# Performance work log

Measured on AMD Instinct MI355X. Metric: run time of the kernel, lower is better.

## Reference

```python
import jax, jax.numpy as jnp
import numpy as np

IN, H, T = 512, 1024, 1024


def _xavier(key, shape):
    a = (6.0 / (shape[0] + shape[1])) ** 0.5
    return jax.random.uniform(key, shape, minval=-a, maxval=a, dtype=jnp.float32)


def setup_inputs() -> dict:
    key = jax.random.key(0)
    ks = jax.random.split(key, 20)
    inp = {
        'x': jax.random.normal(ks[0], (1, T, IN), dtype=jnp.float32),
        'time': jax.random.uniform(ks[1], (T,), dtype=jnp.float32),
    }
    # initial states ~ N(0, 0.1) as in the source forward
    names = ['h0_1', 'c0_1', 'h0_2', 'c0_2', 'h0_3', 'c0_3']
    for i, n in enumerate(names):
        inp[n] = 0.1 * jax.random.normal(ks[2 + i], (1, H), dtype=jnp.float32)
    # LSTMCell params: weights xavier_uniform, biases uniform(0,1) (torch gate order i,f,g,o)
    inp['W_ih1'] = _xavier(ks[8], (4 * H, IN + 1))
    inp['W_hh1'] = _xavier(ks[9], (4 * H, H))
    inp['b_ih1'] = jax.random.uniform(ks[10], (4 * H,), dtype=jnp.float32)
    inp['b_hh1'] = jax.random.uniform(ks[11], (4 * H,), dtype=jnp.float32)
    inp['W_ih2'] = _xavier(ks[12], (4 * H, H))
    inp['W_hh2'] = _xavier(ks[13], (4 * H, H))
    inp['b_ih2'] = jax.random.uniform(ks[14], (4 * H,), dtype=jnp.float32)
    inp['b_hh2'] = jax.random.uniform(ks[15], (4 * H,), dtype=jnp.float32)
    return inp


def reference(x, time, h0_1, c0_1, h0_2, c0_2, h0_3, c0_3,
              W_ih1, W_hh1, b_ih1, b_hh1, W_ih2, W_hh2, b_ih2, b_hh2):
    def cell(xt, h, c, W_ih, W_hh, b_ih, b_hh):
        gates = xt @ W_ih.T + b_ih + h @ W_hh.T + b_hh  # (1, 4H)
        i, f, g, o = jnp.split(gates, 4, axis=-1)
        c_new = jax.nn.sigmoid(f) * c + jax.nn.sigmoid(i) * jnp.tanh(g)
        h_new = jax.nn.sigmoid(o) * jnp.tanh(c_new)
        return h_new, c_new

    xs = jnp.concatenate([x[0], time[:, None]], axis=1)  # (T, IN+1)

    def step(carry, xt):
        h1, c1, h2, c2, h3, c3 = carry
        h1, c1 = cell(xt[None, :], h1, c1, W_ih1, W_hh1, b_ih1, b_hh1)
        h2, c2 = cell(h1, h2, c2, W_ih2, W_hh2, b_ih2, b_hh2)
        # source calls self.lstm2 again for the third layer (lstm3 unused)
        h3, c3 = cell(h2, h3, c3, W_ih2, W_hh2, b_ih2, b_hh2)
        return (h1, c1, h2, c2, h3, c3), h3[0]

    carry, hs = jax.lax.scan(step, (h0_1, c0_1, h0_2, c0_2, h0_3, c0_3), xs)
    hs = hs[None]              # (1, T, H)
    h_final = carry[4]         # (1, H) -- last h3
    attn = jnp.einsum('bth,bh->bt', hs, h_final)
    w = jax.nn.softmax(attn, axis=1)
    context = jnp.einsum('bth,bt->bh', hs, w)  # (1, H)
    return context
```

## Files before the change

### kernel.cpp

```cpp
#include <hip/hip_runtime.h>
#include <hip/hip_fp16.h>

#define TSTEPS 1024
#define HDIM   1024
#define INDIM  512
#define NGATE  4096
#define NWG_L1  64
#define NWG_L23 128
#define NWG_TOT 192
#define POISON_U 0x7C7C7C7Cu
#define SPIN_MAX (1 << 20)


typedef _Float16 half2v __attribute__((ext_vector_type(2)));
typedef decltype(__builtin_amdgcn_cvt_pkrtz(0.f, 0.f)) f16x2b;

#define PINU(v) asm volatile("" : "+v"(v))

#if defined(__has_builtin)
#if __has_builtin(__builtin_amdgcn_fdot2)
#define HAVE_FDOT2 1
#endif
#endif

#ifdef HAVE_FDOT2
__device__ __forceinline__ float dot2f(unsigned h, unsigned w, float c) {
    return __builtin_amdgcn_fdot2(__builtin_bit_cast(f16x2b, h),
                                  __builtin_bit_cast(f16x2b, w), c, false);
}
#else
__device__ __forceinline__ float dot2f(unsigned h, unsigned w, float c) {
    half2v a = __builtin_bit_cast(half2v, h);
    half2v b = __builtin_bit_cast(half2v, w);
    c = fmaf((float)a[0], (float)b[0], c);
    c = fmaf((float)a[1], (float)b[1], c);
    return c;
}
#endif

__device__ __forceinline__ float wave_sum64_dpp(float v) {
    int x;
    x = __builtin_amdgcn_update_dpp(0, __float_as_int(v), 0x111, 0xf, 0xf, false); v += __int_as_float(x);
    x = __builtin_amdgcn_update_dpp(0, __float_as_int(v), 0x112, 0xf, 0xf, false); v += __int_as_float(x);
    x = __builtin_amdgcn_update_dpp(0, __float_as_int(v), 0x114, 0xf, 0xf, false); v += __int_as_float(x);
    x = __builtin_amdgcn_update_dpp(0, __float_as_int(v), 0x118, 0xf, 0xf, false); v += __int_as_float(x);
    x = __builtin_amdgcn_update_dpp(0, __float_as_int(v), 0x142, 0xa, 0xf, false); v += __int_as_float(x);
    x = __builtin_amdgcn_update_dpp(0, __float_as_int(v), 0x143, 0xc, 0xf, false); v += __int_as_float(x);
    return v;
}

__device__ __forceinline__ float sigm(float x) { return 1.f / (1.f + __expf(-x)); }
__device__ __forceinline__ float fast_tanh(float x) {
    float t = __expf(-2.f * fabsf(x));
    float r = (1.f - t) / (1.f + t);
    return copysignf(r, x);
}

__device__ __forceinline__ unsigned pack_h(float a, float b) {
    auto p = __builtin_amdgcn_cvt_pkrtz(a, b);
    return __builtin_bit_cast(unsigned, p);
}

__device__ __forceinline__ unsigned agent_loadu(const unsigned* p) {
    return __hip_atomic_load(const_cast<unsigned*>(p), __ATOMIC_RELAXED,
                             __HIP_MEMORY_SCOPE_AGENT);
}
__device__ __forceinline__ void agent_storeu(unsigned* p, unsigned v) {
    __hip_atomic_store(p, v, __ATOMIC_RELAXED, __HIP_MEMORY_SCOPE_AGENT);
}
__device__ __forceinline__ float agent_loadf(const float* p) {
    return __hip_atomic_load(const_cast<float*>(p), __ATOMIC_RELAXED,
                             __HIP_MEMORY_SCOPE_AGENT);
}
__device__ __forceinline__ void agent_storef(float* p, float v) {
    __hip_atomic_store(p, v, __ATOMIC_RELAXED, __HIP_MEMORY_SCOPE_AGENT);
}
__device__ __forceinline__ bool isp(float v) { return __float_as_uint(v) == POISON_U; }

__device__ __forceinline__ void grid_barrier(int* bar, int idx, int tid) {
    __syncthreads();
    if (tid == 0) {
        __hip_atomic_fetch_add(&bar[idx], 1, __ATOMIC_ACQ_REL,
                               __HIP_MEMORY_SCOPE_AGENT);
        for (int it = 0; it < SPIN_MAX; ++it) {
            if (__hip_atomic_load(&bar[idx], __ATOMIC_ACQUIRE,
                                  __HIP_MEMORY_SCOPE_AGENT) >= NWG_TOT) break;
            __builtin_amdgcn_s_sleep(2);
        }
    }
    __syncthreads();
}

#define BM 64
#define BN 64
#define BK 32
#define GK (INDIM + 1)

__device__ __forceinline__ void gemm_tile(
    int bm, int bn, int ttid,
    const float* __restrict__ B, const float* __restrict__ bias1,
    const float* __restrict__ bias2, float* C,
    const float* __restrict__ x, const float* __restrict__ timev,
    float (*As)[BM + 1], float (*Bs)[BN + 1])
{
    const int t0 = bm * BM;
    const int n0 = bn * BN;
    const int tx = ttid & 15;
    const int ty = ttid >> 4;

    float acc[4][4] = {{0.f}};

    for (int kc = 0; kc < GK; kc += BK) {
#pragma unroll
        for (int i = 0; i < 8; i++) {
            int idx = ttid + i * 256;
            int r = idx >> 5;
            int c = idx & 31;
            int col = kc + c;
            int trow = t0 + r;
            float av = (col < INDIM) ? x[(size_t)trow * INDIM + col]
                                     : ((col == INDIM) ? timev[trow] : 0.f);
            As[c][r] = av;
            int nrow = n0 + r;
            Bs[c][r] = (col < GK) ? B[(size_t)nrow * GK + col] : 0.f;
        }
        __syncthreads();

#pragma unroll
        for (int kk = 0; kk < BK; kk++) {
            float a[4], b[4];
#pragma unroll
            for (int i = 0; i < 4; i++) a[i] = As[kk][ty * 4 + i];
#pragma unroll
            for (int j = 0; j < 4; j++) b[j] = Bs[kk][tx * 4 + j];
#pragma unroll
            for (int i = 0; i < 4; i++)
#pragma unroll
                for (int j = 0; j < 4; j++)
                    acc[i][j] = fmaf(a[i], b[j], acc[i][j]);
        }
        __syncthreads();
    }

#pragma unroll
    for (int i = 0; i < 4; i++) {
        int trow = t0 + ty * 4 + i;
#pragma unroll
        for (int j = 0; j < 4; j++) {
            int n = n0 + tx * 4 + j;
            agent_storef(C + (size_t)trow * NGATE + n,
                         acc[i][j] + bias1[n] + bias2[n]);
        }
    }
}

__global__ __launch_bounds__(1024, 4) void fused_scan(
    const float* __restrict__ Whh1,
    float* G1,
    const float* __restrict__ Wih2,
    const float* __restrict__ Whh2,
    const float* __restrict__ Wih1,
    const float* __restrict__ bih1, const float* __restrict__ bhh1,
    const float* __restrict__ xin, const float* __restrict__ timev,
    const float* bih2, const float* bhh2,
    const float* h0_1, const float* c0_1,
    const float* h0_2, const float* c0_2,
    const float* h0_3, const float* c0_3,
    unsigned* H1p, unsigned* H2p, unsigned* H3p,
    float* H3f,
    float* attnb, float* outp, int* bar)
{
    __shared__ unsigned shp1[512];
    __shared__ unsigned shp2[512];
    __shared__ unsigned shp3[512];
    __shared__ float gbuf[16][4];
    __shared__ float AsT[4][BK][BM + 1];
    __shared__ float BsT[4][BK][BN + 1];

    const int tid = threadIdx.x;
    const int wg  = blockIdx.x;
    const int q   = tid >> 6;
    const int s   = tid & 63;

    if (wg < NWG_L1) {
        const int u0 = wg << 4;
        const int u  = u0 + q;
        unsigned w[4][8];
#pragma unroll
        for (int g = 0; g < 4; ++g) {
            const float* row = Whh1 + (size_t)((g << 10) + u) * 1024 + 2 * s;
#pragma unroll
            for (int m = 0; m < 8; ++m) {
                float2 v = *(const float2*)(row + 128 * m);
                w[g][m] = pack_h(v.x, v.y);
            }
        }
        float c1 = (tid < 16) ? c0_1[u0 + tid] : 0.f;
        unsigned pv = 0u;

        for (int t = 0; t < TSTEPS; ++t) {
#pragma unroll
            for (int g = 0; g < 4; ++g)
#pragma unroll
                for (int m = 0; m < 8; ++m) PINU(w[g][m]);

            float Gv0 = 0.f, Gv1 = 0.f, Gv2 = 0.f, Gv3 = 0.f;
            if (tid < 16) {
                const float* gptr = G1 + (size_t)t * NGATE + u0 + tid;
                Gv0 = agent_loadf(gptr);
                Gv1 = agent_loadf(gptr + 1024);
                Gv2 = agent_loadf(gptr + 2048);
                Gv3 = agent_loadf(gptr + 3072);
            }
            if (tid < 512) {
                if (t == 0) {
                    shp1[tid] = pack_h(h0_1[2 * tid], h0_1[2 * tid + 1]);
                } else {
                    const unsigned* p = H1p + (size_t)(t - 1) * 512 + tid;
                    unsigned v = pv;
                    for (int it = 0; it < SPIN_MAX; ++it) {
                        if (__ballot(v == POISON_U) == 0ULL) break;
                        __builtin_amdgcn_s_sleep(1);
                        if (v == POISON_U) v = agent_loadu(p);
                    }
                    shp1[tid] = v;
                }
            }
            __syncthreads();

            float a0 = 0.f, a1 = 0.f, a2 = 0.f, a3 = 0.f;
#pragma unroll
            for (int m = 0; m < 8; ++m) {
                unsigned hu = shp1[s + 64 * m];
                a0 = dot2f(hu, w[0][m], a0);
                a1 = dot2f(hu, w[1][m], a1);
                a2 = dot2f(hu, w[2][m], a2);
                a3 = dot2f(hu, w[3][m], a3);
            }
            a0 = wave_sum64_dpp(a0);
            a1 = wave_sum64_dpp(a1);
            a2 = wave_sum64_dpp(a2);
            a3 = wave_sum64_dpp(a3);
            if (s == 63) {
                gbuf[q][0] = a0;
                gbuf[q][1] = a1;
                gbuf[q][2] = a2;
                gbuf[q][3] = a3;
            }
            __syncthreads();

            if (tid < 16) {
                const float* gptr = G1 + (size_t)t * NGATE + u0 + tid;
                for (int it = 0; it < SPIN_MAX; ++it) {
                    if (__ballot(isp(Gv0) | isp(Gv1) | isp(Gv2) | isp(Gv3)) == 0ULL)
                        break;
                    __builtin_amdgcn_s_sleep(1);
                    if (isp(Gv0)) Gv0 = agent_loadf(gptr);
                    if (isp(Gv1)) Gv1 = agent_loadf(gptr + 1024);
                    if (isp(Gv2)) Gv2 = agent_loadf(gptr + 2048);
                    if (isp(Gv3)) Gv3 = agent_loadf(gptr + 3072);
                }
                float gi = gbuf[tid][0] + Gv0;
                float gf = gbuf[tid][1] + Gv1;
                float gg = gbuf[tid][2] + Gv2;
                float go = gbuf[tid][3] + Gv3;
                float i_ = sigm(gi), f_ = sigm(gf), g_ = fast_tanh(gg), o_ = sigm(go);
                c1 = f_ * c1 + i_ * g_;
                float hn = o_ * fast_tanh(c1);
                float hnn = __shfl_down(hn, 1, 64);
                if (!(tid & 1))
                    agent_storeu(H1p + (size_t)t * 512 + (u0 >> 1) + (tid >> 1),
                                 pack_h(hn, hnn));
            }
            if (tid < 512 && t < TSTEPS - 1) {
                pv = agent_loadu(H1p + (size_t)t * 512 + tid);
                PINU(pv);
            }
        }
    } else {
        {
            const int team = tid >> 8;
            const int ttid = tid & 255;
            const int tg   = (wg - NWG_L1) * 4 + team;
#pragma unroll
            for (int r = 0; r < 2; ++r) {
                const int wk = tg + r * 512;
                gemm_tile(wk >> 6, wk & 63, ttid, Wih1, bih1, bhh1, G1,
                          xin, timev, AsT[team], BsT[team]);
            }
        }
        __syncthreads();

        const int ul = q >> 1;
        const int gp = q & 1;
        const int u0 = (wg - NWG_L1) << 3;
        const int u  = u0 + ul;
        unsigned wi[2][8], wh[2][8];
#pragma unroll
        for (int j = 0; j < 2; ++j) {
            const float* ri = Wih2 + (size_t)(((2 * gp + j) << 10) + u) * 1024 + 2 * s;
            const float* rh = Whh2 + (size_t)(((2 * gp + j) << 10) + u) * 1024 + 2 * s;
#pragma unroll
            for (int m = 0; m < 8; ++m) {
                float2 vi = *(const float2*)(ri + 128 * m);
                float2 vh = *(const float2*)(rh + 128 * m);
                wi[j][m] = pack_h(vi.x, vi.y);
                wh[j][m] = pack_h(vh.x, vh.y);
            }
        }
        float bias0 = 0.f, bias1v = 0.f, bias2v = 0.f, bias3 = 0.f, cst = 0.f;
        if (tid < 16) {
            int uu = u0 + (tid & 7);
            bias0  = bih2[uu]        + bhh2[uu];
            bias1v = bih2[1024 + uu] + bhh2[1024 + uu];
            bias2v = bih2[2048 + uu] + bhh2[2048 + uu];
            bias3  = bih2[3072 + uu] + bhh2[3072 + uu];
            cst = (tid < 8) ? c0_2[u0 + tid] : c0_3[u0 + tid - 8];
        }
        unsigned pv1 = 0u;
        if (tid < 512) pv1 = agent_loadu(H1p + tid);

        for (int t = 0; t <= TSTEPS; ++t) {
#pragma unroll
            for (int j = 0; j < 2; ++j)
#pragma unroll
                for (int m = 0; m < 8; ++m) { PINU(wi[j][m]); PINU(wh[j][m]); }

            const bool do2 = (t < TSTEPS);
            const bool do3 = (t >= 1);

            if (tid < 512 && do2) {
                const unsigned* p = H1p + (size_t)t * 512 + tid;
                unsigned v = pv1;
                for (int it = 0; it < SPIN_MAX; ++it) {
                    if (__ballot(v == POISON_U) == 0ULL) break;
                    __builtin_amdgcn_s_sleep(1);
                    if (v == POISON_U) v = agent_loadu(p);
                }
                shp1[tid] = v;
            }
            __syncthreads();

            float p20 = 0.f, p21 = 0.f;
#pragma unroll
            for (int m = 0; m < 8; ++m) {
                unsigned h1u = shp1[s + 64 * m];
                p20 = dot2f(h1u, wi[0][m], p20);
                p21 = dot2f(h1u, wi[1][m], p21);
            }

            if (tid < 512) {
                if (t == 0) {
                    shp2[tid] = pack_h(h0_2[2 * tid], h0_2[2 * tid + 1]);
                } else {
                    const unsigned* p = H2p + (size_t)(t - 1) * 512 + tid;
                    unsigned v = agent_loadu(p);
                    for (int it = 0; it < SPIN_MAX; ++it) {
                        if (__ballot(v == POISON_U) == 0ULL) break;
                        __builtin_amdgcn_s_sleep(1);
                        if (v == POISON_U) v = agent_loadu(p);
                    }
                    shp2[tid] = v;
                }
            } else {
                const int sid = tid - 512;
                if (t == 1) {
                    shp3[sid] = pack_h(h0_3[2 * sid], h0_3[2 * sid + 1]);
                } else if (t > 1) {
                    const unsigned* p = H3p + (size_t)(t - 2) * 512 + sid;
                    unsigned v = agent_loadu(p);
                    for (int it = 0; it < SPIN_MAX; ++it) {
                        if (__ballot(v == POISON_U) == 0ULL) break;
                        __builtin_amdgcn_s_sleep(1);
                        if (v == POISON_U) v = agent_loadu(p);
                    }
                    shp3[sid] = v;
                }
            }
            __syncthreads();

            float p30 = 0.f, p31 = 0.f;
#pragma unroll
            for (int m = 0; m < 8; ++m) {
                unsigned h2u = shp2[s + 64 * m];
                unsigned h3u = shp3[s + 64 * m];
                p20 = dot2f(h2u, wh[0][m], p20);
                p21 = dot2f(h2u, wh[1][m], p21);
                p30 = dot2f(h2u, wi[0][m], p30);
                p31 = dot2f(h2u, wi[1][m], p31);
                p30 = dot2f(h3u, wh[0][m], p30);
                p31 = dot2f(h3u, wh[1][m], p31);
            }
            float s20 = wave_sum64_dpp(p20);
            float s21 = wave_sum64_dpp(p21);
            float s30 = wave_sum64_dpp(p30);
            float s31 = wave_sum64_dpp(p31);
            if (s == 63) {
                gbuf[ul][2 * gp]          = s20;
                gbuf[ul][2 * gp + 1]      = s21;
                gbuf[8 + ul][2 * gp]      = s30;
                gbuf[8 + ul][2 * gp + 1]  = s31;
            }
            __syncthreads();

            if (tid < 16) {
                const bool act = (tid < 8) ? do2 : do3;
                float hn = 0.f;
                if (act) {
                    float gi = gbuf[tid][0] + bias0;
                    float gf = gbuf[tid][1] + bias1v;
                    float gg = gbuf[tid][2] + bias2v;
                    float go = gbuf[tid][3] + bias3;
                    float i_ = sigm(gi), f_ = sigm(gf), g_ = fast_tanh(gg), o_ = sigm(go);
                    cst = f_ * cst + i_ * g_;
                    hn = o_ * fast_tanh(cst);
                }
                float hnn = __shfl_down(hn, 1, 64);
                if (act) {
                    if (tid < 8) {
                        if (!(tid & 1))
                            agent_storeu(H2p + (size_t)t * 512 + (u0 >> 1) + (tid >> 1),
                                         pack_h(hn, hnn));
                    } else {
                        if (!(tid & 1))
                            agent_storeu(H3p + (size_t)(t - 1) * 512 + (u0 >> 1) + ((tid - 8) >> 1),
                                         pack_h(hn, hnn));
                        agent_storef(H3f + (size_t)(t - 1) * HDIM + u0 + (tid - 8), hn);
                    }
                }
            }
            if (tid < 512 && t < TSTEPS - 1) {
                pv1 = agent_loadu(H1p + (size_t)(t + 1) * 512 + tid);
                PINU(pv1);
            }
        }
    }

    const int gw = wg * 16 + q;
    grid_barrier(bar, 0, tid);

    if (gw < TSTEPS) {
        const float* hrow = H3f + (size_t)gw * HDIM;
        const float* hf   = H3f + (size_t)(TSTEPS - 1) * HDIM;
        float p = 0.f;
#pragma unroll
        for (int j = 0; j < 16; ++j) {
            int k = s + 64 * j;
            p = fmaf(agent_loadf(hrow + k), agent_loadf(hf + k), p);
        }
        p = wave_sum64_dpp(p);
        if (s == 63) agent_storef(attnb + gw, p);
    }
    grid_barrier(bar, 1, tid);

    if (wg == 0 && tid < 64) {
        float m = -1e30f;
        for (int i = 0; i < 16; ++i)
            m = fmaxf(m, agent_loadf(attnb + tid + i * 64));
#pragma unroll
        for (int d = 32; d; d >>= 1) m = fmaxf(m, __shfl_xor(m, d, 64));
        float ss = 0.f;
        for (int i = 0; i < 16; ++i)
            ss += __expf(agent_loadf(attnb + tid + i * 64) - m);
#pragma unroll
        for (int d = 32; d; d >>= 1) ss += __shfl_xor(ss, d, 64);
        float inv = 1.f / ss;
        for (int i = 0; i < 16; ++i) {
            int idx = tid + i * 64;
            agent_storef(attnb + idx,
                         __expf(agent_loadf(attnb + idx) - m) * inv);
        }
    }
    grid_barrier(bar, 2, tid);

    if (gw < HDIM) {
        float p = 0.f;
#pragma unroll
        for (int j = 0; j < 16; ++j) {
            int t = s + 64 * j;
            p = fmaf(agent_loadf(H3f + (size_t)t * HDIM + gw),
                     agent_loadf(attnb + t), p);
        }
        p = wave_sum64_dpp(p);
        if (s == 63) outp[gw] = p;
    }
}

extern "C" void kernel_launch(void* const* d_in, const int* in_sizes, int n_in,
                              void* d_out, int out_size, void* d_ws, size_t ws_size,
                              hipStream_t stream)
{
    const float* x     = (const float*)d_in[0];
    const float* timev = (const float*)d_in[1];
    const float* h0_1  = (const float*)d_in[2];
    const float* c0_1  = (const float*)d_in[3];
    const float* h0_2  = (const float*)d_in[4];
    const float* c0_2  = (const float*)d_in[5];
    const float* h0_3  = (const float*)d_in[6];
    const float* c0_3  = (const float*)d_in[7];
    const float* Wih1  = (const float*)d_in[8];
    const float* Whh1  = (const float*)d_in[9];
    const float* bih1  = (const float*)d_in[10];
    const float* bhh1  = (const float*)d_in[11];
    const float* Wih2  = (const float*)d_in[12];
    const float* Whh2  = (const float*)d_in[13];
    const float* bih2  = (const float*)d_in[14];
    const float* bhh2  = (const float*)d_in[15];

    float* G      = (float*)d_ws;
    unsigned* H1p = (unsigned*)(G + (size_t)TSTEPS * NGATE);
    unsigned* H2p = H1p + (size_t)TSTEPS * 512;
    unsigned* H3p = H2p + (size_t)TSTEPS * 512;
    float* H3f    = (float*)(H3p + (size_t)TSTEPS * 512);
    float* attnb  = H3f + (size_t)TSTEPS * HDIM;
    int* bar      = (int*)(attnb + 1024);
    float* out    = (float*)d_out;

    hipMemsetAsync(G, 0x7C,
                   (size_t)TSTEPS * NGATE * sizeof(float) +
                   (size_t)3 * TSTEPS * 512 * sizeof(unsigned), stream);
    hipMemsetAsync(bar, 0, 16 * sizeof(int), stream);

    {
        const float* a0 = Whh1;  float* a1 = G;
        const float* a2 = Wih2;  const float* a3 = Whh2;
        const float* a4 = Wih1;  const float* a5 = bih1;  const float* a6 = bhh1;
        const float* a7 = x;     const float* a8 = timev;
        const float* a9 = bih2;  const float* a10 = bhh2;
        const float* a11 = h0_1; const float* a12 = c0_1;
        const float* a13 = h0_2; const float* a14 = c0_2;
        const float* a15 = h0_3; const float* a16 = c0_3;
        unsigned* a17 = H1p; unsigned* a18 = H2p; unsigned* a19 = H3p;
        float* a20 = H3f; float* a21 = attnb; float* a22 = out; int* a23 = bar;
        void* args[] = {&a0,&a1,&a2,&a3,&a4,&a5,&a6,&a7,&a8,&a9,&a10,&a11,
                        &a12,&a13,&a14,&a15,&a16,&a17,&a18,&a19,&a20,&a21,
                        &a22,&a23};
        hipLaunchCooperativeKernel((void*)fused_scan, dim3(NWG_TOT), dim3(1024),
                                   args, 0, stream);
    }
}
```

Before: 2.892 ms.

## Split layer-2/3 step phases, fuse softmax into context, pad LDS tiles

Splits the layer-2 and layer-3 computation inside each timestep so layer 2's hidden state is computed and published before layer 3's dot products, which shortens the critical path for the next step's dependency. It also removes one grid barrier by having every wave redundantly compute the softmax max and sum and fold the normalisation into the context reduction. LDS tile padding changes from +1 to +4, and weight packing switches to round-to-nearest fp16. The costs are an extra __syncthreads per step and redundant softmax work in every wave.

```diff
diff --git a/kernel.cpp b/kernel.cpp
--- a/kernel.cpp
+++ b/kernel.cpp
@@ -60,6 +60,10 @@
     auto p = __builtin_amdgcn_cvt_pkrtz(a, b);
     return __builtin_bit_cast(unsigned, p);
 }
+__device__ __forceinline__ unsigned pack_rne(float a, float b) {
+    return (unsigned)__half_as_ushort(__float2half(a)) |
+           ((unsigned)__half_as_ushort(__float2half(b)) << 16);
+}
 
 __device__ __forceinline__ unsigned agent_loadu(const unsigned* p) {
     return __hip_atomic_load(const_cast<unsigned*>(p), __ATOMIC_RELAXED,
@@ -101,7 +105,7 @@
     const float* __restrict__ B, const float* __restrict__ bias1,
     const float* __restrict__ bias2, float* C,
     const float* __restrict__ x, const float* __restrict__ timev,
-    float (*As)[BM + 1], float (*Bs)[BN + 1])
+    float (*As)[BM + 4], float (*Bs)[BN + 4])
 {
     const int t0 = bm * BM;
     const int n0 = bn * BN;
@@ -174,8 +178,8 @@
     __shared__ unsigned shp2[512];
     __shared__ unsigned shp3[512];
     __shared__ float gbuf[16][4];
-    __shared__ float AsT[4][BK][BM + 1];
-    __shared__ float BsT[4][BK][BN + 1];
+    __shared__ float AsT[4][BK][BM + 4];
+    __shared__ float BsT[4][BK][BN + 4];
 
     const int tid = threadIdx.x;
     const int wg  = blockIdx.x;
@@ -192,7 +196,7 @@
 #pragma unroll
             for (int m = 0; m < 8; ++m) {
                 float2 v = *(const float2*)(row + 128 * m);
-                w[g][m] = pack_h(v.x, v.y);
+                w[g][m] = pack_rne(v.x, v.y);
             }
         }
         float c1 = (tid < 16) ? c0_1[u0 + tid] : 0.f;
@@ -304,8 +308,8 @@
             for (int m = 0; m < 8; ++m) {
                 float2 vi = *(const float2*)(ri + 128 * m);
                 float2 vh = *(const float2*)(rh + 128 * m);
-                wi[j][m] = pack_h(vi.x, vi.y);
-                wh[j][m] = pack_h(vh.x, vh.y);
+                wi[j][m] = pack_rne(vi.x, vi.y);
+                wh[j][m] = pack_rne(vh.x, vh.y);
             }
         }
         float bias0 = 0.f, bias1v = 0.f, bias2v = 0.f, bias3 = 0.f, cst = 0.f;
@@ -379,55 +383,65 @@
             }
             __syncthreads();
 
+#pragma unroll
+            for (int m = 0; m < 8; ++m) {
+                unsigned h2u = shp2[s + 64 * m];
+                p20 = dot2f(h2u, wh[0][m], p20);
+                p21 = dot2f(h2u, wh[1][m], p21);
+            }
+            float s20 = wave_sum64_dpp(p20);
+            float s21 = wave_sum64_dpp(p21);
+            if (s == 63) {
+                gbuf[ul][2 * gp]     = s20;
+                gbuf[ul][2 * gp + 1] = s21;
+            }
+            __syncthreads();
+
+            if (tid < 8 && do2) {
+                float gi = gbuf[tid][0] + bias0;
+                float gf = gbuf[tid][1] + bias1v;
+                float gg = gbuf[tid][2] + bias2v;
+                float go = gbuf[tid][3] + bias3;
+                float i_ = sigm(gi), f_ = sigm(gf), g_ = fast_tanh(gg), o_ = sigm(go);
+                cst = f_ * cst + i_ * g_;
+                float hn = o_ * fast_tanh(cst);
+                float hnn = __shfl_down(hn, 1, 64);
+                if (!(tid & 1))
+                    agent_storeu(H2p + (size_t)t * 512 + (u0 >> 1) + (tid >> 1),
+                                 pack_h(hn, hnn));
+            }
+
             float p30 = 0.f, p31 = 0.f;
 #pragma unroll
             for (int m = 0; m < 8; ++m) {
                 unsigned h2u = shp2[s + 64 * m];
                 unsigned h3u = shp3[s + 64 * m];
-                p20 = dot2f(h2u, wh[0][m], p20);
-                p21 = dot2f(h2u, wh[1][m], p21);
                 p30 = dot2f(h2u, wi[0][m], p30);
                 p31 = dot2f(h2u, wi[1][m], p31);
                 p30 = dot2f(h3u, wh[0][m], p30);
                 p31 = dot2f(h3u, wh[1][m], p31);
             }
-            float s20 = wave_sum64_dpp(p20);
-            float s21 = wave_sum64_dpp(p21);
             float s30 = wave_sum64_dpp(p30);
             float s31 = wave_sum64_dpp(p31);
             if (s == 63) {
-                gbuf[ul][2 * gp]          = s20;
-                gbuf[ul][2 * gp + 1]      = s21;
-                gbuf[8 + ul][2 * gp]      = s30;
-                gbuf[8 + ul][2 * gp + 1]  = s31;
+                gbuf[8 + ul][2 * gp]     = s30;
+                gbuf[8 + ul][2 * gp + 1] = s31;
             }
             __syncthreads();
 
-            if (tid < 16) {
-                const bool act = (tid < 8) ? do2 : do3;
-                float hn = 0.f;
-                if (act) {
-                    float gi = gbuf[tid][0] + bias0;
-                    float gf = gbuf[tid][1] + bias1v;
-                    float gg = gbuf[tid][2] + bias2v;
-                    float go = gbuf[tid][3] + bias3;
-                    float i_ = sigm(gi), f_ = sigm(gf), g_ = fast_tanh(gg), o_ = sigm(go);
-                    cst = f_ * cst + i_ * g_;
-                    hn = o_ * fast_tanh(cst);
-                }
+            if (tid >= 8 && tid < 16 && do3) {
+                float gi = gbuf[tid][0] + bias0;
+                float gf = gbuf[tid][1] + bias1v;
+                float gg = gbuf[tid][2] + bias2v;
+                float go = gbuf[tid][3] + bias3;
+                float i_ = sigm(gi), f_ = sigm(gf), g_ = fast_tanh(gg), o_ = sigm(go);
+                cst = f_ * cst + i_ * g_;
+                float hn = o_ * fast_tanh(cst);
                 float hnn = __shfl_down(hn, 1, 64);
-                if (act) {
-                    if (tid < 8) {
-                        if (!(tid & 1))
-                            agent_storeu(H2p + (size_t)t * 512 + (u0 >> 1) + (tid >> 1),
-                                         pack_h(hn, hnn));
-                    } else {
-                        if (!(tid & 1))
-                            agent_storeu(H3p + (size_t)(t - 1) * 512 + (u0 >> 1) + ((tid - 8) >> 1),
-                                         pack_h(hn, hnn));
-                        agent_storef(H3f + (size_t)(t - 1) * HDIM + u0 + (tid - 8), hn);
-                    }
-                }
+                if (!(tid & 1))
+                    agent_storeu(H3p + (size_t)(t - 1) * 512 + (u0 >> 1) + ((tid - 8) >> 1),
+                                 pack_h(hn, hnn));
+                agent_storef(H3f + (size_t)(t - 1) * HDIM + u0 + (tid - 8), hn);
             }
             if (tid < 512 && t < TSTEPS - 1) {
                 pv1 = agent_loadu(H1p + (size_t)(t + 1) * 512 + tid);
@@ -453,36 +467,27 @@
     }
     grid_barrier(bar, 1, tid);
 
-    if (wg == 0 && tid < 64) {
+    if (gw < HDIM) {
+        float av[16];
         float m = -1e30f;
-        for (int i = 0; i < 16; ++i)
-            m = fmaxf(m, agent_loadf(attnb + tid + i * 64));
+#pragma unroll
+        for (int j = 0; j < 16; ++j) {
+            av[j] = agent_loadf(attnb + s + 64 * j);
+            m = fmaxf(m, av[j]);
+        }
 #pragma unroll
         for (int d = 32; d; d >>= 1) m = fmaxf(m, __shfl_xor(m, d, 64));
-        float ss = 0.f;
-        for (int i = 0; i < 16; ++i)
-            ss += __expf(agent_loadf(attnb + tid + i * 64) - m);
-#pragma unroll
-        for (int d = 32; d; d >>= 1) ss += __shfl_xor(ss, d, 64);
-        float inv = 1.f / ss;
-        for (int i = 0; i < 16; ++i) {
-            int idx = tid + i * 64;
-            agent_storef(attnb + idx,
-                         __expf(agent_loadf(attnb + idx) - m) * inv);
-        }
-    }
-    grid_barrier(bar, 2, tid);
-
-    if (gw < HDIM) {
-        float p = 0.f;
+        float S = 0.f, p = 0.f;
 #pragma unroll
         for (int j = 0; j < 16; ++j) {
             int t = s + 64 * j;
-            p = fmaf(agent_loadf(H3f + (size_t)t * HDIM + gw),
-                     agent_loadf(attnb + t), p);
-        }
+            float e = __expf(av[j] - m);
+            S += e;
+            p = fmaf(e, agent_loadf(H3f + (size_t)t * HDIM + gw), p);
+        }
+        S = wave_sum64_dpp(S);
         p = wave_sum64_dpp(p);
-        if (s == 63) outp[gw] = p;
+        if (s == 63) outp[gw] = p / S;
     }
 }
 
```

Result: slower. 2.996 ms (+3.6%).
